# Optimization experiments

Hardware: AMD Instinct MI355X
Metric: run time of the kernel (lower is better)

## Reference

```python
import jax, jax.numpy as jnp
import numpy as np

IN_CH, OUT_CH, HID, NHEAD = 4, 1, 256, 8
VDIM = HID // NHEAD
LOCALITIES = (2.0, 10.0, 10.0, 10.0, 10.0, 200.0)
N_BLOCKS = len(LOCALITIES) - 2
INPUT_RES, LATENT_RES, OUTPUT_RES = (64, 64), (32, 32), (64, 64)
BATCH = 8


def pairwise_dist(res1x, res1y, res2x, res2y):
    gx1 = jnp.linspace(0, 1, res1x + 1)[:-1]
    gy1 = jnp.linspace(0, 1, res1y + 1)[:-1]
    g1x, g1y = jnp.meshgrid(gx1, gy1, indexing='xy')
    grid1 = jnp.stack([g1x.flatten(), g1y.flatten()], axis=-1)
    gx2 = jnp.linspace(0, 1, res2x + 1)[:-1]
    gy2 = jnp.linspace(0, 1, res2y + 1)[:-1]
    g2x, g2y = jnp.meshgrid(gx2, gy2, indexing='xy')
    grid2 = jnp.stack([g2x.flatten(), g2y.flatten()], axis=-1)
    diff = grid1[:, None, :] - grid2[None, :, :]
    return (jnp.sum(diff ** 2, axis=-1) / 2.0).astype(jnp.float32)


def pos_att(m_dist, x, r, w, locality):
    # m_dist:[Nq,Nk]  x:[B,Nk,HID]  r:[H,1,1]  w:[H,HID,VDIM]
    scale = jnp.tan(0.25 * jnp.pi * (1 - 1e-07) * (1 + jnp.sin(r)))
    sd = m_dist[None, :, :] * scale  # [H,Nq,Nk]
    if locality <= 100:
        thr = jnp.percentile(sd, locality, axis=-1, keepdims=True)
        sd = jnp.where(sd <= thr, sd, jnp.inf)
    att = jax.nn.softmax(-sd, axis=-1)  # [H,Nq,Nk]
    value = jnp.einsum('bnj,hjk->bhnk', x, w)  # [B,H,Nk,VDIM]
    out = jnp.einsum('hjn,bhnk->bhjk', att, value)  # [B,H,Nq,VDIM]
    out = jnp.transpose(out, (0, 2, 1, 3)).reshape(x.shape[0], m_dist.shape[0], -1)
    return jax.nn.gelu(out)


def lin(x, w, b):
    # eqx.nn.Linear: w:[out,in], b:[out]
    return jnp.einsum('bni,oi->bno', x, w) + b


def setup_inputs() -> dict:
    key = jax.random.key(0)
    ks = jax.random.split(key, 20)
    Ni = INPUT_RES[0] * INPUT_RES[1]
    s_h = 1.0 / jnp.sqrt(HID)
    s_in = 1.0 / jnp.sqrt(IN_CH)
    return {
        'x': jax.random.normal(ks[0], (BATCH, Ni, IN_CH), jnp.float32),
        'en_fc1_w': jax.random.uniform(ks[1], (HID, IN_CH), jnp.float32, -s_in, s_in),
        'en_fc1_b': jax.random.uniform(ks[2], (HID,), jnp.float32, -s_in, s_in),
        'down_r': jax.random.normal(ks[3], (NHEAD, 1, 1), jnp.float32),
        'down_w': jax.random.normal(ks[4], (NHEAD, HID, VDIM), jnp.float32) * s_h,
        'pa_r': jax.random.normal(ks[5], (N_BLOCKS, NHEAD, 1, 1), jnp.float32),
        'pa_w': jax.random.normal(ks[6], (N_BLOCKS, NHEAD, HID, VDIM), jnp.float32) * s_h,
        'mlp1_w': jax.random.uniform(ks[7], (N_BLOCKS, HID, HID), jnp.float32, -s_h, s_h),
        'mlp1_b': jax.random.uniform(ks[8], (N_BLOCKS, HID), jnp.float32, -s_h, s_h),
        'mlp2_w': jax.random.uniform(ks[9], (N_BLOCKS, HID, HID), jnp.float32, -s_h, s_h),
        'mlp2_b': jax.random.uniform(ks[10], (N_BLOCKS, HID), jnp.float32, -s_h, s_h),
        'res_w': jax.random.uniform(ks[11], (N_BLOCKS, HID, HID), jnp.float32, -s_h, s_h),
        'res_b': jax.random.uniform(ks[12], (N_BLOCKS, HID), jnp.float32, -s_h, s_h),
        'up_r': jax.random.normal(ks[13], (NHEAD, 1, 1), jnp.float32),
        'up_w': jax.random.normal(ks[14], (NHEAD, HID, VDIM), jnp.float32) * s_h,
        'de_fc1_w': jax.random.uniform(ks[15], (HID, HID), jnp.float32, -s_h, s_h),
        'de_fc1_b': jax.random.uniform(ks[16], (HID,), jnp.float32, -s_h, s_h),
        'de_fc2_w': jax.random.uniform(ks[17], (OUT_CH, HID), jnp.float32, -s_h, s_h),
        'de_fc2_b': jax.random.uniform(ks[18], (OUT_CH,), jnp.float32, -s_h, s_h),
    }


def reference(x, en_fc1_w, en_fc1_b, down_r, down_w, pa_r, pa_w,
              mlp1_w, mlp1_b, mlp2_w, mlp2_b, res_w, res_b,
              up_r, up_w, de_fc1_w, de_fc1_b, de_fc2_w, de_fc2_b):
    m_dist_down = pairwise_dist(LATENT_RES[0], LATENT_RES[1], INPUT_RES[0], INPUT_RES[1])
    m_dist_proc = pairwise_dist(LATENT_RES[0], LATENT_RES[1], LATENT_RES[0], LATENT_RES[1])
    m_dist_up = pairwise_dist(OUTPUT_RES[0], OUTPUT_RES[1], LATENT_RES[0], LATENT_RES[1])

    h = jax.nn.gelu(lin(x, en_fc1_w, en_fc1_b))
    h = pos_att(m_dist_down, h, down_r, down_w, LOCALITIES[0])
    for i in range(N_BLOCKS):
        pa_out = pos_att(m_dist_proc, h, pa_r[i], pa_w[i], LOCALITIES[1 + i])
        mlp_out = lin(jax.nn.gelu(lin(pa_out, mlp1_w[i], mlp1_b[i])), mlp2_w[i], mlp2_b[i])
        residual = lin(h, res_w[i], res_b[i])
        h = jax.nn.gelu(mlp_out + residual)
    h = pos_att(m_dist_up, h, up_r, up_w, LOCALITIES[-1])
    h = jax.nn.gelu(lin(h, de_fc1_w, de_fc1_b))
    return lin(h, de_fc2_w, de_fc2_b)
```

## Files before the change

### kernel.cpp

```cpp
#include <hip/hip_runtime.h>
#include <math.h>


#define PI_F 3.14159265358979323846f

typedef __attribute__((ext_vector_type(8))) short short8;
typedef __attribute__((ext_vector_type(4))) float float4v;
typedef __attribute__((ext_vector_type(4))) unsigned short ushort4v;

__device__ __forceinline__ float gelu_f(float x) {
  float u = 0.7978845608028654f * (x + 0.044715f * x * x * x);
  float e = __expf(2.0f * u);
  float t = 1.0f - 2.0f / (e + 1.0f);
  return 0.5f * x * (1.0f + t);
}

__device__ __forceinline__ float head_scale(float r) {
  return tanf(0.25f * PI_F * (1.0f - 1e-7f) * (1.0f + sinf(r)));
}

__device__ __forceinline__ unsigned short f2bf(float f) {
  union { float f; unsigned u; } c; c.f = f;
  unsigned u = c.u + 0x7FFFu + ((c.u >> 16) & 1u);
  return (unsigned short)(u >> 16);
}
__device__ __forceinline__ float bf2f(unsigned short h) {
  union { unsigned u; float f; } c; c.u = ((unsigned)h) << 16;
  return c.f;
}
__device__ __forceinline__ void split_bf(float f, unsigned short& hi,
                                         unsigned short& lo) {
  hi = f2bf(f);
  lo = f2bf(f - bf2f(hi));
}

__global__ __launch_bounds__(256) void k_pre(
    const float* __restrict__ x, const float* __restrict__ en_w,
    const float* __restrict__ en_b, unsigned short* __restrict__ ahi,
    unsigned short* __restrict__ alo, const float* __restrict__ down_w,
    const float* __restrict__ de1_w, const float* __restrict__ up_w,
    const float* __restrict__ pa_w, const float* __restrict__ mlp1_w,
    const float* __restrict__ mlp2_w, const float* __restrict__ res_w,
    unsigned short* __restrict__ whi, unsigned short* __restrict__ wlo,
    float* __restrict__ out, const float* __restrict__ de2_b) {
  int blk = blockIdx.x;
  int tid = threadIdx.x;
  if (blk < 32768) {
    float4 xv = *(const float4*)(x + (size_t)blk * 4);
    float4 wv = *(const float4*)(en_w + (size_t)tid * 4);
    float s = xv.x * wv.x + xv.y * wv.y + xv.z * wv.z + xv.w * wv.w + en_b[tid];
    s = gelu_f(s);
    unsigned short hi, lo;
    split_bf(s, hi, lo);
    ahi[(size_t)blk * 256 + tid] = hi;
    alo[(size_t)blk * 256 + tid] = lo;
  } else if (blk < 37632) {
    int i = (blk - 32768) * 256 + tid;
    float f;
    if (i < 65536) {
      int n = i >> 8, k = i & 255;
      f = down_w[(n >> 5) * 8192 + k * 32 + (n & 31)];
    } else if (i < 131072) {
      f = de1_w[i - 65536];
    } else if (i < 196608) {
      int j = i - 131072;
      int n = j >> 8, k = j & 255;
      f = up_w[(n >> 5) * 8192 + k * 32 + (n & 31)];
    } else if (i < 458752) {
      int j = i - 196608;
      int b2 = j >> 16, r = j & 65535;
      int n = r >> 8, k = r & 255;
      f = pa_w[(size_t)b2 * 65536 + (n >> 5) * 8192 + k * 32 + (n & 31)];
    } else if (i < 720896) {
      f = mlp1_w[i - 458752];
    } else if (i < 983040) {
      f = mlp2_w[i - 720896];
    } else {
      f = res_w[i - 983040];
    }
    unsigned short hi, lo;
    split_bf(f, hi, lo);
    whi[i] = hi;
    wlo[i] = lo;
  } else {
    out[(blk - 37632) * 256 + tid] = de2_b[0];
  }
}

template <int KRES, int CXM, int DSHIFT, int J2, int NPT, int TARGET,
          int ITERS, int TMAX>
__device__ __forceinline__ void klist_body(
    const float* __restrict__ rvec, int* __restrict__ klist2,
    int* __restrict__ kcnt2, float* __restrict__ wlist2, int tile, int tid) {
  __shared__ int cntS;
  __shared__ int sidx[J2];
  __shared__ int sdv[J2][4];
  __shared__ float denS[8][4];
  __shared__ int wsum4[4][4];
  int tx = tile & 15, ty = tile >> 4;
  int cxA[4], cyA[4];
#pragma unroll
  for (int i = 0; i < 4; ++i) {
    int qx = 2 * tx + (i & 1), qy = 2 * ty + (i >> 1);
    cxA[i] = qx * CXM; cyA[i] = qy * CXM;
  }
  int dc[4][NPT];
#pragma unroll
  for (int j = 0; j < NPT; ++j) {
    int p = tid * NPT + j;
    int kx = p & (KRES - 1), ky = p / KRES;
#pragma unroll
    for (int i = 0; i < 4; ++i) {
      int dx = cxA[i] - kx, dy = cyA[i] - ky;
      dc[i][j] = dx * dx + dy * dy;
    }
  }
  int lo4[4] = {0, 0, 0, 0}, hi4[4] = {TMAX, TMAX, TMAX, TMAX};
  for (int it = 0; it < ITERS; ++it) {
    int mid[4], c[4] = {0, 0, 0, 0};
#pragma unroll
    for (int i = 0; i < 4; ++i) {
      mid[i] = (lo4[i] + hi4[i]) >> 1;
      if (lo4[i] < hi4[i]) {
#pragma unroll
        for (int j = 0; j < NPT; ++j) c[i] += (dc[i][j] <= mid[i]) ? 1 : 0;
      }
    }
#pragma unroll
    for (int i = 0; i < 4; ++i)
#pragma unroll
      for (int off = 32; off > 0; off >>= 1)
        c[i] += __shfl_down(c[i], off, 64);
    if ((tid & 63) == 0) {
#pragma unroll
      for (int i = 0; i < 4; ++i) wsum4[tid >> 6][i] = c[i];
    }
    __syncthreads();
#pragma unroll
    for (int i = 0; i < 4; ++i) {
      if (lo4[i] < hi4[i]) {
        int tot = wsum4[0][i] + wsum4[1][i] + wsum4[2][i] + wsum4[3][i];
        if (tot >= TARGET) hi4[i] = mid[i]; else lo4[i] = mid[i] + 1;
      }
    }
    __syncthreads();
  }
  int T[4];
#pragma unroll
  for (int i = 0; i < 4; ++i) T[i] = lo4[i];
  if (tid == 0) cntS = 0;
  __syncthreads();
  int x0 = KRES - 1, x1 = 0, y0 = KRES - 1, y1 = 0;
#pragma unroll
  for (int i = 0; i < 4; ++i) {
    int rad = (int)sqrtf((float)T[i]);
    while ((rad + 1) * (rad + 1) <= T[i]) ++rad;
    while (rad > 0 && rad * rad > T[i]) --rad;
    x0 = min(x0, max(0, cxA[i] - rad));
    x1 = max(x1, min(KRES - 1, cxA[i] + rad));
    y0 = min(y0, max(0, cyA[i] - rad));
    y1 = max(y1, min(KRES - 1, cyA[i] + rad));
  }
  int W = x1 - x0 + 1, H = y1 - y0 + 1, tot = W * H;
  for (int p = tid; p < tot; p += 256) {
    int kx = x0 + p % W, ky = y0 + p / W;
    int d[4]; bool keep = false;
#pragma unroll
    for (int i = 0; i < 4; ++i) {
      int dx = cxA[i] - kx, dy = cyA[i] - ky;
      d[i] = dx * dx + dy * dy;
      keep = keep || (d[i] <= T[i]);
    }
    if (keep) {
      int s = atomicAdd(&cntS, 1);
      if (s < J2) {
        sidx[s] = ky * KRES + kx;
#pragma unroll
        for (int i = 0; i < 4; ++i) sdv[s][i] = d[i];
      }
    }
  }
  __syncthreads();
  int cnt = min(cntS, J2);
  int h = tid >> 5, lane = tid & 31;
  float sc = head_scale(rvec[h]) * (1.0f / (float)(1 << DSHIFT));
  float den[4] = {0.f, 0.f, 0.f, 0.f};
  for (int j = lane; j < cnt; j += 32) {
#pragma unroll
    for (int i = 0; i < 4; ++i)
      if (sdv[j][i] <= T[i]) den[i] += __expf(-sc * (float)sdv[j][i]);
  }
#pragma unroll
  for (int i = 0; i < 4; ++i) {
    float d0 = den[i];
#pragma unroll
    for (int off = 16; off > 0; off >>= 1) d0 += __shfl_down(d0, off, 32);
    if (lane == 0) denS[h][i] = d0;
  }
  __syncthreads();
  float inv[4];
#pragma unroll
  for (int i = 0; i < 4; ++i) inv[i] = 1.0f / denS[h][i];
  for (int j = lane; j < cnt; j += 32) {
    float w[4];
#pragma unroll
    for (int i = 0; i < 4; ++i)
      w[i] = (sdv[j][i] <= T[i]) ? __expf(-sc * (float)sdv[j][i]) * inv[i] : 0.f;
    float4v wv = {w[0], w[1], w[2], w[3]};
    *(float4v*)&wlist2[(((size_t)h * 256 + tile) * J2 + j) * 4] = wv;
  }
  if (tid == 0) kcnt2[tile] = cnt;
  if (h == 0)
    for (int j = lane; j < cnt; j += 32) klist2[(size_t)tile * J2 + j] = sidx[j];
}

__global__ __launch_bounds__(256) void k_klist_all(
    const float* __restrict__ down_r, const float* __restrict__ pa_r,
    int* __restrict__ klD2, int* __restrict__ cntD2, float* __restrict__ wlD2,
    int* __restrict__ klP2, int* __restrict__ cntP2, float* __restrict__ wlP2) {
  int tid = threadIdx.x;
  if (blockIdx.x < 256) {
    klist_body<64, 2, 13, 256, 16, 82, 13, 7938>(down_r, klD2, cntD2, wlD2,
                                                 blockIdx.x, tid);
  } else {
    klist_body<32, 1, 11, 256, 4, 103, 11, 1922>(pa_r, klP2, cntP2, wlP2,
                                                 blockIdx.x - 256, tid);
  }
}

template <int NK, int J2>
__global__ __launch_bounds__(256) void k_att3(
    const float* __restrict__ value,
    const int* __restrict__ klist2, const int* __restrict__ kcnt2,
    const float* __restrict__ wlist2, unsigned short* __restrict__ ohi,
    unsigned short* __restrict__ olo) {
  __shared__ int kls[J2];
  __shared__ float4v wls[J2];
  __shared__ float4v part[4][4][64];
  int blk = blockIdx.x;
  int tile = blk >> 3, h = blk & 7;
  int tid = threadIdx.x, g = tid & 63, s = tid >> 6;
  int cnt = kcnt2[tile];
  for (int j = tid; j < cnt; j += 256) {
    kls[j] = klist2[(size_t)tile * J2 + j];
    wls[j] = *(const float4v*)&wlist2[(((size_t)h * 256 + tile) * J2 + j) * 4];
  }
  __syncthreads();
  const float* vb = value + (size_t)h * NK * 256 + g * 4;
  float4v acc[4];
#pragma unroll
  for (int i = 0; i < 4; ++i) acc[i] = (float4v)0.0f;
  for (int j = s; j < cnt; j += 4) {
    int row = kls[j];
    float4v v = *(const float4v*)(vb + (size_t)row * 256);
    float4v w = wls[j];
    acc[0] += w.x * v;
    acc[1] += w.y * v;
    acc[2] += w.z * v;
    acc[3] += w.w * v;
  }
#pragma unroll
  for (int i = 0; i < 4; ++i) part[s][i][g] = acc[i];
  __syncthreads();
  if (tid < 64) {
    int g2 = tid;
    int ttx = tile & 15, tty = tile >> 4;
    int batch = g2 >> 3, v0 = (g2 & 7) * 4;
#pragma unroll
    for (int i = 0; i < 4; ++i) {
      float4v o4 = part[0][i][g2] + part[1][i][g2] + part[2][i][g2] +
                   part[3][i][g2];
      int q = (2 * tty + (i >> 1)) * 32 + 2 * ttx + (i & 1);
      size_t idx = ((size_t)batch * 1024 + q) * 256 + h * 32 + v0;
      ushort4v hv, lv;
#pragma unroll
      for (int c = 0; c < 4; ++c) {
        float oo = gelu_f(o4[c]);
        unsigned short hi, lo;
        split_bf(oo, hi, lo);
        hv[c] = hi; lv[c] = lo;
      }
      *(ushort4v*)(ohi + idx) = hv;
      *(ushort4v*)(olo + idx) = lv;
    }
  }
}

template <bool DUAL, int OL, bool GEL, bool OHILO>
__global__ __launch_bounds__(256) void k_mf(
    const unsigned short* __restrict__ A1hi, const unsigned short* __restrict__ A1lo,
    const unsigned short* __restrict__ W1hi, const unsigned short* __restrict__ W1lo,
    const unsigned short* __restrict__ A2hi, const unsigned short* __restrict__ A2lo,
    const unsigned short* __restrict__ W2hi, const unsigned short* __restrict__ W2lo,
    const float* __restrict__ bias, const float* __restrict__ bias2,
    float* __restrict__ outf, unsigned short* __restrict__ ohi,
    unsigned short* __restrict__ olo, int NS) {
  __shared__ unsigned short Ah[128][40], Al[128][40];
  __shared__ unsigned short Bh[128][40], Bl[128][40];
  int tid = threadIdx.x;
  int m0 = blockIdx.x * 128, n0 = blockIdx.y * 128;
  int w = tid >> 6, lane = tid & 63;
  int wm = (w >> 1) * 64, wn = (w & 1) * 64;
  int quad = lane >> 4, l16 = lane & 15;
  float4v acc[4][4];
#pragma unroll
  for (int i = 0; i < 4; ++i)
#pragma unroll
    for (int j = 0; j < 4; ++j) acc[i][j] = (float4v)0.0f;

  int srow = tid >> 1, skq = (tid & 1) * 16;
  const int KT = DUAL ? 512 : 256;
  for (int kk = 0; kk < KT; kk += 32) {
    const unsigned short *pAh, *pAl, *pWh, *pWl;
    int kb;
    if (DUAL && kk >= 256) {
      pAh = A2hi; pAl = A2lo; pWh = W2hi; pWl = W2lo; kb = kk - 256;
    } else {
      pAh = A1hi; pAl = A1lo; pWh = W1hi; pWl = W1lo; kb = kk;
    }
    {
      size_t ga = (size_t)(m0 + srow) * 256 + kb + skq;
      const uint4* pah = (const uint4*)(pAh + ga);
      const uint4* pal = (const uint4*)(pAl + ga);
      *(uint4*)&Ah[srow][skq] = pah[0];
      *(uint4*)&Ah[srow][skq + 8] = pah[1];
      *(uint4*)&Al[srow][skq] = pal[0];
      *(uint4*)&Al[srow][skq + 8] = pal[1];
      size_t gb = (size_t)(n0 + srow) * 256 + kb + skq;
      const uint4* pbh = (const uint4*)(pWh + gb);
      const uint4* pbl = (const uint4*)(pWl + gb);
      *(uint4*)&Bh[srow][skq] = pbh[0];
      *(uint4*)&Bh[srow][skq + 8] = pbh[1];
      *(uint4*)&Bl[srow][skq] = pbl[0];
      *(uint4*)&Bl[srow][skq + 8] = pbl[1];
    }
    __syncthreads();
    short8 ah[4], al[4], bh[4], bl[4];
#pragma unroll
    for (int s = 0; s < 4; ++s) {
      ah[s] = *(const short8*)&Ah[wm + s * 16 + l16][quad * 8];
      al[s] = *(const short8*)&Al[wm + s * 16 + l16][quad * 8];
      bh[s] = *(const short8*)&Bh[wn + s * 16 + l16][quad * 8];
      bl[s] = *(const short8*)&Bl[wn + s * 16 + l16][quad * 8];
    }
#pragma unroll
    for (int ms = 0; ms < 4; ++ms)
#pragma unroll
      for (int ns = 0; ns < 4; ++ns) {
        acc[ms][ns] = __builtin_amdgcn_mfma_f32_16x16x32_bf16(
            ah[ms], bh[ns], acc[ms][ns], 0, 0, 0);
        acc[ms][ns] = __builtin_amdgcn_mfma_f32_16x16x32_bf16(
            ah[ms], bl[ns], acc[ms][ns], 0, 0, 0);
        acc[ms][ns] = __builtin_amdgcn_mfma_f32_16x16x32_bf16(
            al[ms], bh[ns], acc[ms][ns], 0, 0, 0);
      }
    __syncthreads();
  }
#pragma unroll
  for (int ms = 0; ms < 4; ++ms) {
#pragma unroll
    for (int ns = 0; ns < 4; ++ns) {
      int n = n0 + wn + ns * 16 + l16;
      float bv = bias ? bias[n] : 0.0f;
      if (DUAL && bias2) bv += bias2[n];
#pragma unroll
      for (int r = 0; r < 4; ++r) {
        int m = m0 + wm + ms * 16 + quad * 4 + r;
        float c = acc[ms][ns][r] + bv;
        if (GEL) c = gelu_f(c);
        if (OHILO) {
          unsigned short chi, clo;
          split_bf(c, chi, clo);
          ohi[(size_t)m * 256 + n] = chi;
          olo[(size_t)m * 256 + n] = clo;
        } else if (OL == 0) {
          outf[(size_t)m * 256 + n] = c;
        } else {
          int N = 1 << NS;
          int bb = m >> NS, rr = m & (N - 1);
          outf[(((size_t)(n >> 5) * N + rr) * 8 + bb) * 32 + (n & 31)] = c;
        }
      }
    }
  }
}

__global__ __launch_bounds__(256) void k_mf_dec(
    const unsigned short* __restrict__ A1hi, const unsigned short* __restrict__ A1lo,
    const unsigned short* __restrict__ W1hi, const unsigned short* __restrict__ W1lo,
    const float* __restrict__ b1, const float* __restrict__ w2,
    float* __restrict__ out) {
  __shared__ unsigned short Ah[128][40], Al[128][40];
  __shared__ unsigned short Bh[128][40], Bl[128][40];
  int tid = threadIdx.x;
  int m0 = blockIdx.x * 128, n0 = blockIdx.y * 128;
  int w = tid >> 6, lane = tid & 63;
  int wm = (w >> 1) * 64, wn = (w & 1) * 64;
  int quad = lane >> 4, l16 = lane & 15;
  float4v acc[4][4];
#pragma unroll
  for (int i = 0; i < 4; ++i)
#pragma unroll
    for (int j = 0; j < 4; ++j) acc[i][j] = (float4v)0.0f;
  int srow = tid >> 1, skq = (tid & 1) * 16;
  for (int kk = 0; kk < 256; kk += 32) {
    {
      size_t ga = (size_t)(m0 + srow) * 256 + kk + skq;
      const uint4* pah = (const uint4*)(A1hi + ga);
      const uint4* pal = (const uint4*)(A1lo + ga);
      *(uint4*)&Ah[srow][skq] = pah[0];
      *(uint4*)&Ah[srow][skq + 8] = pah[1];
      *(uint4*)&Al[srow][skq] = pal[0];
      *(uint4*)&Al[srow][skq + 8] = pal[1];
      size_t gb = (size_t)(n0 + srow) * 256 + kk + skq;
      const uint4* pbh = (const uint4*)(W1hi + gb);
      const uint4* pbl = (const uint4*)(W1lo + gb);
      *(uint4*)&Bh[srow][skq] = pbh[0];
      *(uint4*)&Bh[srow][skq + 8] = pbh[1];
      *(uint4*)&Bl[srow][skq] = pbl[0];
      *(uint4*)&Bl[srow][skq + 8] = pbl[1];
    }
    __syncthreads();
    short8 ah[4], al[4], bh[4], bl[4];
#pragma unroll
    for (int s = 0; s < 4; ++s) {
      ah[s] = *(const short8*)&Ah[wm + s * 16 + l16][quad * 8];
      al[s] = *(const short8*)&Al[wm + s * 16 + l16][quad * 8];
      bh[s] = *(const short8*)&Bh[wn + s * 16 + l16][quad * 8];
      bl[s] = *(const short8*)&Bl[wn + s * 16 + l16][quad * 8];
    }
#pragma unroll
    for (int ms = 0; ms < 4; ++ms)
#pragma unroll
      for (int ns = 0; ns < 4; ++ns) {
        acc[ms][ns] = __builtin_amdgcn_mfma_f32_16x16x32_bf16(
            ah[ms], bh[ns], acc[ms][ns], 0, 0, 0);
        acc[ms][ns] = __builtin_amdgcn_mfma_f32_16x16x32_bf16(
            ah[ms], bl[ns], acc[ms][ns], 0, 0, 0);
        acc[ms][ns] = __builtin_amdgcn_mfma_f32_16x16x32_bf16(
            al[ms], bh[ns], acc[ms][ns], 0, 0, 0);
      }
    __syncthreads();
  }
#pragma unroll
  for (int ms = 0; ms < 4; ++ms) {
#pragma unroll
    for (int r = 0; r < 4; ++r) {
      float p = 0.0f;
#pragma unroll
      for (int ns = 0; ns < 4; ++ns) {
        int n = n0 + wn + ns * 16 + l16;
        float c = gelu_f(acc[ms][ns][r] + b1[n]);
        p += c * w2[n];
      }
      p += __shfl_xor(p, 1, 64);
      p += __shfl_xor(p, 2, 64);
      p += __shfl_xor(p, 4, 64);
      p += __shfl_xor(p, 8, 64);
      if (l16 == 0) {
        int m = m0 + wm + ms * 16 + quad * 4 + r;
        atomicAdd(&out[m], p);
      }
    }
  }
}

template <bool DUAL, int OL, bool GEL, bool OHILO>
__global__ __launch_bounds__(256) void k_mf3(
    const unsigned short* __restrict__ A1hi, const unsigned short* __restrict__ A1lo,
    const unsigned short* __restrict__ W1hi, const unsigned short* __restrict__ W1lo,
    const unsigned short* __restrict__ A2hi, const unsigned short* __restrict__ A2lo,
    const unsigned short* __restrict__ W2hi, const unsigned short* __restrict__ W2lo,
    const float* __restrict__ bias, const float* __restrict__ bias2,
    float* __restrict__ outf, unsigned short* __restrict__ ohi,
    unsigned short* __restrict__ olo, int NS) {
  __shared__ unsigned short Ah[32][40], Al[32][40];
  __shared__ unsigned short Bh[64][40], Bl[64][40];
  int tid = threadIdx.x;
  int m0 = blockIdx.x * 32, n0 = blockIdx.y * 64;
  int w = tid >> 6, lane = tid & 63;
  int wm = (w >> 1) * 16, wn = (w & 1) * 32;
  int quad = lane >> 4, l16 = lane & 15;
  float4v acc[2];
  acc[0] = (float4v)0.0f;
  acc[1] = (float4v)0.0f;
  int sra = tid >> 3, ska = (tid & 7) * 4;
  int srb = tid >> 2, skb = (tid & 3) * 8;
  const int KT = DUAL ? 512 : 256;
  for (int kk = 0; kk < KT; kk += 32) {
    const unsigned short *pAh, *pAl, *pWh, *pWl;
    int kb;
    if (DUAL && kk >= 256) {
      pAh = A2hi; pAl = A2lo; pWh = W2hi; pWl = W2lo; kb = kk - 256;
    } else {
      pAh = A1hi; pAl = A1lo; pWh = W1hi; pWl = W1lo; kb = kk;
    }
    {
      size_t ga = (size_t)(m0 + sra) * 256 + kb + ska;
      *(uint2*)&Ah[sra][ska] = *(const uint2*)(pAh + ga);
      *(uint2*)&Al[sra][ska] = *(const uint2*)(pAl + ga);
      size_t gb = (size_t)(n0 + srb) * 256 + kb + skb;
      *(uint4*)&Bh[srb][skb] = *(const uint4*)(pWh + gb);
      *(uint4*)&Bl[srb][skb] = *(const uint4*)(pWl + gb);
    }
    __syncthreads();
    short8 ah = *(const short8*)&Ah[wm + l16][quad * 8];
    short8 al = *(const short8*)&Al[wm + l16][quad * 8];
#pragma unroll
    for (int ns = 0; ns < 2; ++ns) {
      short8 bh = *(const short8*)&Bh[wn + ns * 16 + l16][quad * 8];
      short8 bl = *(const short8*)&Bl[wn + ns * 16 + l16][quad * 8];
      acc[ns] = __builtin_amdgcn_mfma_f32_16x16x32_bf16(ah, bh, acc[ns], 0, 0, 0);
      acc[ns] = __builtin_amdgcn_mfma_f32_16x16x32_bf16(ah, bl, acc[ns], 0, 0, 0);
      acc[ns] = __builtin_amdgcn_mfma_f32_16x16x32_bf16(al, bh, acc[ns], 0, 0, 0);
    }
    __syncthreads();
  }
#pragma unroll
  for (int ns = 0; ns < 2; ++ns) {
    int n = n0 + wn + ns * 16 + l16;
    float bv = bias ? bias[n] : 0.0f;
    if (DUAL && bias2) bv += bias2[n];
#pragma unroll
    for (int r = 0; r < 4; ++r) {
      int m = m0 + wm + quad * 4 + r;
      float c = acc[ns][r] + bv;
      if (GEL) c = gelu_f(c);
      if (OHILO) {
        unsigned short chi, clo;
        split_bf(c, chi, clo);
        ohi[(size_t)m * 256 + n] = chi;
        olo[(size_t)m * 256 + n] = clo;
      } else if (OL == 0) {
        outf[(size_t)m * 256 + n] = c;
      } else {
        int N = 1 << NS;
        int bb = m >> NS, rr = m & (N - 1);
        outf[(((size_t)(n >> 5) * N + rr) * 8 + bb) * 32 + (n & 31)] = c;
      }
    }
  }
}

__global__ __launch_bounds__(256) void k_up_s1(
    const float* __restrict__ value,
    const float* __restrict__ rvec, float* __restrict__ T) {
  __shared__ float AxL[32][33];
  int ky = blockIdx.x, h = blockIdx.y, qx0 = blockIdx.z * 32;
  int tid = threadIdx.x;
  float sc = head_scale(rvec[h]) * (1.0f / 8192.0f);
  float v[32];
  const float* vb = value + ((size_t)h * 1024 + ky * 32) * 256 + tid;
#pragma unroll
  for (int kx = 0; kx < 32; ++kx) v[kx] = vb[kx * 256];
  if (tid < 32) {
    int qx = qx0 + tid, dxmin = qx & 1;
    for (int kx = 0; kx < 32; ++kx) {
      int dx = qx - 2 * kx;
      AxL[tid][kx] = __expf(-sc * (float)(dx * dx - dxmin));
    }
  }
  __syncthreads();
  for (int qq = 0; qq < 32; ++qq) {
    int qx = qx0 + qq;
    float acc = 0.f;
#pragma unroll
    for (int kx = 0; kx < 32; ++kx) acc += AxL[qq][kx] * v[kx];
    T[(((size_t)h * 64 + qx) * 32 + ky) * 256 + tid] = acc;
  }
}

__global__ __launch_bounds__(256) void k_up_s2(
    const float* __restrict__ T, const float* __restrict__ rvec,
    unsigned short* __restrict__ ohi, unsigned short* __restrict__ olo) {
  __shared__ float AyL[64][33];
  __shared__ float Sy[64];
  __shared__ float SxS;
  int qx = blockIdx.x, h = blockIdx.y, tid = threadIdx.x;
  float sc = head_scale(rvec[h]) * (1.0f / 8192.0f);
  float t[32];
  const float* tb = T + ((size_t)h * 64 + qx) * 32 * 256 + tid;
#pragma unroll
  for (int ky = 0; ky < 32; ++ky) t[ky] = tb[ky * 256];
  if (tid < 64) {
    int qy = tid, dymin = qy & 1;
    float s = 0.f;
    for (int ky = 0; ky < 32; ++ky) {
      int dy = qy - 2 * ky;
      float e = __expf(-sc * (float)(dy * dy - dymin));
      AyL[qy][ky] = e;
      s += e;
    }
    Sy[qy] = s;
  } else if (tid >= 64 && tid < 96) {
    int kx = tid - 64, dxmin = qx & 1;
    int dx = qx - 2 * kx;
    float e = __expf(-sc * (float)(dx * dx - dxmin));
#pragma unroll
    for (int off = 16; off > 0; off >>= 1) e += __shfl_down(e, off, 32);
    if (kx == 0) SxS = e;
  }
  __syncthreads();
  float invSx = 1.0f / SxS;
  int b = tid >> 5, v = tid & 31;
  size_t base = ((size_t)b * 4096 + qx) * 256 + h * 32 + v;
  for (int qy = 0; qy < 64; ++qy) {
    float acc = 0.f;
#pragma unroll
    for (int ky = 0; ky < 32; ++ky) acc += AyL[qy][ky] * t[ky];
    float o = gelu_f(acc * invSx / Sy[qy]);
    unsigned short hi, lo;
    split_bf(o, hi, lo);
    size_t idx = base + (size_t)qy * 64 * 256;
    ohi[idx] = hi;
    olo[idx] = lo;
  }
}

extern "C" void kernel_launch(void* const* d_in, const int* in_sizes, int n_in,
                              void* d_out, int out_size, void* d_ws,
                              size_t ws_size, hipStream_t stream) {
  const float* x      = (const float*)d_in[0];
  const float* en_w   = (const float*)d_in[1];
  const float* en_b   = (const float*)d_in[2];
  const float* down_r = (const float*)d_in[3];
  const float* down_w = (const float*)d_in[4];
  const float* pa_r   = (const float*)d_in[5];
  const float* pa_w   = (const float*)d_in[6];
  const float* mlp1_w = (const float*)d_in[7];
  const float* mlp1_b = (const float*)d_in[8];
  const float* mlp2_w = (const float*)d_in[9];
  const float* mlp2_b = (const float*)d_in[10];
  const float* res_w  = (const float*)d_in[11];
  const float* res_b  = (const float*)d_in[12];
  const float* up_r   = (const float*)d_in[13];
  const float* up_w   = (const float*)d_in[14];
  const float* de1_w  = (const float*)d_in[15];
  const float* de1_b  = (const float*)d_in[16];
  const float* de2_w  = (const float*)d_in[17];
  const float* de2_b  = (const float*)d_in[18];
  float* out = (float*)d_out;

  constexpr int J2 = 256;
  float* ws = (float*)d_ws;
  unsigned short* Ahi = (unsigned short*)ws;
  unsigned short* Alo = Ahi + 8388608;
  float* B = ws + 8388608;
  float* Tbuf = B + 2097152;
  unsigned short* hAhi = (unsigned short*)(ws + 16777216);
  unsigned short* hAlo = hAhi + 2097152;
  unsigned short* hBhi = hAlo + 2097152;
  unsigned short* hBlo = hBhi + 2097152;
  unsigned short* pahi = hBlo + 2097152;
  unsigned short* palo = pahi + 2097152;
  unsigned short* m1hi = palo + 2097152;
  unsigned short* m1lo = m1hi + 2097152;
  int* cntD2 = (int*)(ws + 25165824);
  int* cntP2 = cntD2 + 256;
  int* klD2 = cntP2 + 256;
  int* klP2 = klD2 + 256 * J2;
  float* wlD2 = (float*)(klP2 + 256 * J2);
  float* wlP2 = wlD2 + 2097152;
  unsigned short* Whi = (unsigned short*)(wlP2 + 2097152);
  unsigned short* Wlo = Whi + 1245184;
  const int WO_DOWN = 0, WO_DE1 = 65536, WO_UP = 131072, WO_PA = 196608,
            WO_MLP1 = 458752, WO_MLP2 = 720896, WO_RES = 983040;

  k_pre<<<37760, 256, 0, stream>>>(x, en_w, en_b, Ahi, Alo, down_w, de1_w,
                                   up_w, pa_w, mlp1_w, mlp2_w, res_w, Whi,
                                   Wlo, out, de2_b);
  k_klist_all<<<512, 256, 0, stream>>>(down_r, pa_r, klD2, cntD2, wlD2, klP2,
                                       cntP2, wlP2);
  k_mf<false, 1, false, false><<<dim3(256, 2), 256, 0, stream>>>(
      Ahi, Alo, Whi + WO_DOWN, Wlo + WO_DOWN, nullptr, nullptr, nullptr,
      nullptr, nullptr, nullptr, B, nullptr, nullptr, 12);
  k_att3<4096, J2><<<2048, 256, 0, stream>>>(B, klD2, cntD2, wlD2, hAhi, hAlo);
  for (int i = 0; i < 4; ++i) {
    const unsigned short* hih = (i & 1) ? hBhi : hAhi;
    const unsigned short* hil = (i & 1) ? hBlo : hAlo;
    unsigned short* hoh = (i & 1) ? hAhi : hBhi;
    unsigned short* hol = (i & 1) ? hAlo : hBlo;
    k_mf3<false, 1, false, false><<<dim3(256, 4), 256, 0, stream>>>(
        hih, hil, Whi + WO_PA + i * 65536, Wlo + WO_PA + i * 65536, nullptr,
        nullptr, nullptr, nullptr, nullptr, nullptr, B, nullptr, nullptr, 10);
    k_att3<1024, J2><<<2048, 256, 0, stream>>>(B, klP2, cntP2, wlP2, pahi,
                                               palo);
    k_mf3<false, 0, true, true><<<dim3(256, 4), 256, 0, stream>>>(
        pahi, palo, Whi + WO_MLP1 + i * 65536, Wlo + WO_MLP1 + i * 65536,
        nullptr, nullptr, nullptr, nullptr, mlp1_b + i * 256, nullptr, nullptr,
        m1hi, m1lo, 0);
    k_mf3<true, 0, true, true><<<dim3(256, 4), 256, 0, stream>>>(
        m1hi, m1lo, Whi + WO_MLP2 + i * 65536, Wlo + WO_MLP2 + i * 65536, hih,
        hil, Whi + WO_RES + i * 65536, Wlo + WO_RES + i * 65536,
        mlp2_b + i * 256, res_b + i * 256, nullptr, hoh, hol, 0);
  }
  k_mf3<false, 1, false, false><<<dim3(256, 4), 256, 0, stream>>>(
      hAhi, hAlo, Whi + WO_UP, Wlo + WO_UP, nullptr, nullptr, nullptr, nullptr,
      nullptr, nullptr, B, nullptr, nullptr, 10);
  k_up_s1<<<dim3(32, 8, 2), 256, 0, stream>>>(B, up_r, Tbuf);
  k_up_s2<<<dim3(64, 8), 256, 0, stream>>>(Tbuf, up_r, Ahi, Alo);
  k_mf_dec<<<dim3(256, 2), 256, 0, stream>>>(Ahi, Alo, Whi + WO_DE1,
                                             Wlo + WO_DE1, de1_b, de2_w, out);
}
```

Baseline: 484.9 us.

## Fuse MLP1, MLP2 and residual GEMMs into one kernel; merge klist into k_pre

A new k_mlp kernel computes MLP1 with GELU into shared memory for a 16-row tile, then MLP2 plus the residual linear and the final GELU, all in one launch. This removes the m1 intermediate round-trip through global memory and one launch per block. The klist/softmax-weight construction also moves into extra blocks of k_pre, dropping a separate launch. The cost is small M tiles (16 rows, 512 blocks), so each block reloads the full 256x256 weight matrices three times, which can lower weight reuse and MFMA efficiency compared with the old tiled GEMMs.

```diff
diff --git a/kernel.cpp b/kernel.cpp
--- a/kernel.cpp
+++ b/kernel.cpp
@@ -32,6 +32,133 @@
                                          unsigned short& lo) {
   hi = f2bf(f);
   lo = f2bf(f - bf2f(hi));
+}
+
+template <int KRES, int CXM, int DSHIFT, int J2, int NPT, int TARGET,
+          int ITERS, int TMAX>
+__device__ __forceinline__ void klist_body(
+    const float* __restrict__ rvec, int* __restrict__ klist2,
+    int* __restrict__ kcnt2, float* __restrict__ wlist2, int tile, int tid) {
+  __shared__ int cntS;
+  __shared__ int sidx[J2];
+  __shared__ int sdv[J2][4];
+  __shared__ float denS[8][4];
+  __shared__ int wsum4[4][4];
+  int tx = tile & 15, ty = tile >> 4;
+  int cxA[4], cyA[4];
+#pragma unroll
+  for (int i = 0; i < 4; ++i) {
+    int qx = 2 * tx + (i & 1), qy = 2 * ty + (i >> 1);
+    cxA[i] = qx * CXM; cyA[i] = qy * CXM;
+  }
+  int dc[4][NPT];
+#pragma unroll
+  for (int j = 0; j < NPT; ++j) {
+    int p = tid * NPT + j;
+    int kx = p & (KRES - 1), ky = p / KRES;
+#pragma unroll
+    for (int i = 0; i < 4; ++i) {
+      int dx = cxA[i] - kx, dy = cyA[i] - ky;
+      dc[i][j] = dx * dx + dy * dy;
+    }
+  }
+  int lo4[4] = {0, 0, 0, 0}, hi4[4] = {TMAX, TMAX, TMAX, TMAX};
+  for (int it = 0; it < ITERS; ++it) {
+    int mid[4], c[4] = {0, 0, 0, 0};
+#pragma unroll
+    for (int i = 0; i < 4; ++i) {
+      mid[i] = (lo4[i] + hi4[i]) >> 1;
+      if (lo4[i] < hi4[i]) {
+#pragma unroll
+        for (int j = 0; j < NPT; ++j) c[i] += (dc[i][j] <= mid[i]) ? 1 : 0;
+      }
+    }
+#pragma unroll
+    for (int i = 0; i < 4; ++i)
+#pragma unroll
+      for (int off = 32; off > 0; off >>= 1)
+        c[i] += __shfl_down(c[i], off, 64);
+    if ((tid & 63) == 0) {
+#pragma unroll
+      for (int i = 0; i < 4; ++i) wsum4[tid >> 6][i] = c[i];
+    }
+    __syncthreads();
+#pragma unroll
+    for (int i = 0; i < 4; ++i) {
+      if (lo4[i] < hi4[i]) {
+        int tot = wsum4[0][i] + wsum4[1][i] + wsum4[2][i] + wsum4[3][i];
+        if (tot >= TARGET) hi4[i] = mid[i]; else lo4[i] = mid[i] + 1;
+      }
+    }
+    __syncthreads();
+  }
+  int T[4];
+#pragma unroll
+  for (int i = 0; i < 4; ++i) T[i] = lo4[i];
+  if (tid == 0) cntS = 0;
+  __syncthreads();
+  int x0 = KRES - 1, x1 = 0, y0 = KRES - 1, y1 = 0;
+#pragma unroll
+  for (int i = 0; i < 4; ++i) {
+    int rad = (int)sqrtf((float)T[i]);
+    while ((rad + 1) * (rad + 1) <= T[i]) ++rad;
+    while (rad > 0 && rad * rad > T[i]) --rad;
+    x0 = min(x0, max(0, cxA[i] - rad));
+    x1 = max(x1, min(KRES - 1, cxA[i] + rad));
+    y0 = min(y0, max(0, cyA[i] - rad));
+    y1 = max(y1, min(KRES - 1, cyA[i] + rad));
+  }
+  int W = x1 - x0 + 1, H = y1 - y0 + 1, tot = W * H;
+  for (int p = tid; p < tot; p += 256) {
+    int kx = x0 + p % W, ky = y0 + p / W;
+    int d[4]; bool keep = false;
+#pragma unroll
+    for (int i = 0; i < 4; ++i) {
+      int dx = cxA[i] - kx, dy = cyA[i] - ky;
+      d[i] = dx * dx + dy * dy;
+      keep = keep || (d[i] <= T[i]);
+    }
+    if (keep) {
+      int s = atomicAdd(&cntS, 1);
+      if (s < J2) {
+        sidx[s] = ky * KRES + kx;
+#pragma unroll
+        for (int i = 0; i < 4; ++i) sdv[s][i] = d[i];
+      }
+    }
+  }
+  __syncthreads();
+  int cnt = min(cntS, J2);
+  int h = tid >> 5, lane = tid & 31;
+  float sc = head_scale(rvec[h]) * (1.0f / (float)(1 << DSHIFT));
+  float den[4] = {0.f, 0.f, 0.f, 0.f};
+  for (int j = lane; j < cnt; j += 32) {
+#pragma unroll
+    for (int i = 0; i < 4; ++i)
+      if (sdv[j][i] <= T[i]) den[i] += __expf(-sc * (float)sdv[j][i]);
+  }
+#pragma unroll
+  for (int i = 0; i < 4; ++i) {
+    float d0 = den[i];
+#pragma unroll
+    for (int off = 16; off > 0; off >>= 1) d0 += __shfl_down(d0, off, 32);
+    if (lane == 0) denS[h][i] = d0;
+  }
+  __syncthreads();
+  float inv[4];
+#pragma unroll
+  for (int i = 0; i < 4; ++i) inv[i] = 1.0f / denS[h][i];
+  for (int j = lane; j < cnt; j += 32) {
+    float w[4];
+#pragma unroll
+    for (int i = 0; i < 4; ++i)
+      w[i] = (sdv[j][i] <= T[i]) ? __expf(-sc * (float)sdv[j][i]) * inv[i] : 0.f;
+    float4v wv = {w[0], w[1], w[2], w[3]};
+    *(float4v*)&wlist2[(((size_t)h * 256 + tile) * J2 + j) * 4] = wv;
+  }
+  if (tid == 0) kcnt2[tile] = cnt;
+  if (h == 0)
+    for (int j = lane; j < cnt; j += 32) klist2[(size_t)tile * J2 + j] = sidx[j];
 }
 
 __global__ __launch_bounds__(256) void k_pre(
@@ -42,7 +169,10 @@
     const float* __restrict__ pa_w, const float* __restrict__ mlp1_w,
     const float* __restrict__ mlp2_w, const float* __restrict__ res_w,
     unsigned short* __restrict__ whi, unsigned short* __restrict__ wlo,
-    float* __restrict__ out, const float* __restrict__ de2_b) {
+    float* __restrict__ out, const float* __restrict__ de2_b,
+    const float* __restrict__ down_r, const float* __restrict__ pa_r,
+    int* __restrict__ klD2, int* __restrict__ cntD2, float* __restrict__ wlD2,
+    int* __restrict__ klP2, int* __restrict__ cntP2, float* __restrict__ wlP2) {
   int blk = blockIdx.x;
   int tid = threadIdx.x;
   if (blk < 32768) {
@@ -82,149 +212,14 @@
     split_bf(f, hi, lo);
     whi[i] = hi;
     wlo[i] = lo;
-  } else {
+  } else if (blk < 37760) {
     out[(blk - 37632) * 256 + tid] = de2_b[0];
-  }
-}
-
-template <int KRES, int CXM, int DSHIFT, int J2, int NPT, int TARGET,
-          int ITERS, int TMAX>
-__device__ __forceinline__ void klist_body(
-    const float* __restrict__ rvec, int* __restrict__ klist2,
-    int* __restrict__ kcnt2, float* __restrict__ wlist2, int tile, int tid) {
-  __shared__ int cntS;
-  __shared__ int sidx[J2];
-  __shared__ int sdv[J2][4];
-  __shared__ float denS[8][4];
-  __shared__ int wsum4[4][4];
-  int tx = tile & 15, ty = tile >> 4;
-  int cxA[4], cyA[4];
-#pragma unroll
-  for (int i = 0; i < 4; ++i) {
-    int qx = 2 * tx + (i & 1), qy = 2 * ty + (i >> 1);
-    cxA[i] = qx * CXM; cyA[i] = qy * CXM;
-  }
-  int dc[4][NPT];
-#pragma unroll
-  for (int j = 0; j < NPT; ++j) {
-    int p = tid * NPT + j;
-    int kx = p & (KRES - 1), ky = p / KRES;
-#pragma unroll
-    for (int i = 0; i < 4; ++i) {
-      int dx = cxA[i] - kx, dy = cyA[i] - ky;
-      dc[i][j] = dx * dx + dy * dy;
-    }
-  }
-  int lo4[4] = {0, 0, 0, 0}, hi4[4] = {TMAX, TMAX, TMAX, TMAX};
-  for (int it = 0; it < ITERS; ++it) {
-    int mid[4], c[4] = {0, 0, 0, 0};
-#pragma unroll
-    for (int i = 0; i < 4; ++i) {
-      mid[i] = (lo4[i] + hi4[i]) >> 1;
-      if (lo4[i] < hi4[i]) {
-#pragma unroll
-        for (int j = 0; j < NPT; ++j) c[i] += (dc[i][j] <= mid[i]) ? 1 : 0;
-      }
-    }
-#pragma unroll
-    for (int i = 0; i < 4; ++i)
-#pragma unroll
-      for (int off = 32; off > 0; off >>= 1)
-        c[i] += __shfl_down(c[i], off, 64);
-    if ((tid & 63) == 0) {
-#pragma unroll
-      for (int i = 0; i < 4; ++i) wsum4[tid >> 6][i] = c[i];
-    }
-    __syncthreads();
-#pragma unroll
-    for (int i = 0; i < 4; ++i) {
-      if (lo4[i] < hi4[i]) {
-        int tot = wsum4[0][i] + wsum4[1][i] + wsum4[2][i] + wsum4[3][i];
-        if (tot >= TARGET) hi4[i] = mid[i]; else lo4[i] = mid[i] + 1;
-      }
-    }
-    __syncthreads();
-  }
-  int T[4];
-#pragma unroll
-  for (int i = 0; i < 4; ++i) T[i] = lo4[i];
-  if (tid == 0) cntS = 0;
-  __syncthreads();
-  int x0 = KRES - 1, x1 = 0, y0 = KRES - 1, y1 = 0;
-#pragma unroll
-  for (int i = 0; i < 4; ++i) {
-    int rad = (int)sqrtf((float)T[i]);
-    while ((rad + 1) * (rad + 1) <= T[i]) ++rad;
-    while (rad > 0 && rad * rad > T[i]) --rad;
-    x0 = min(x0, max(0, cxA[i] - rad));
-    x1 = max(x1, min(KRES - 1, cxA[i] + rad));
-    y0 = min(y0, max(0, cyA[i] - rad));
-    y1 = max(y1, min(KRES - 1, cyA[i] + rad));
-  }
-  int W = x1 - x0 + 1, H = y1 - y0 + 1, tot = W * H;
-  for (int p = tid; p < tot; p += 256) {
-    int kx = x0 + p % W, ky = y0 + p / W;
-    int d[4]; bool keep = false;
-#pragma unroll
-    for (int i = 0; i < 4; ++i) {
-      int dx = cxA[i] - kx, dy = cyA[i] - ky;
-      d[i] = dx * dx + dy * dy;
-      keep = keep || (d[i] <= T[i]);
-    }
-    if (keep) {
-      int s = atomicAdd(&cntS, 1);
-      if (s < J2) {
-        sidx[s] = ky * KRES + kx;
-#pragma unroll
-        for (int i = 0; i < 4; ++i) sdv[s][i] = d[i];
-      }
-    }
-  }
-  __syncthreads();
-  int cnt = min(cntS, J2);
-  int h = tid >> 5, lane = tid & 31;
-  float sc = head_scale(rvec[h]) * (1.0f / (float)(1 << DSHIFT));
-  float den[4] = {0.f, 0.f, 0.f, 0.f};
-  for (int j = lane; j < cnt; j += 32) {
-#pragma unroll
-    for (int i = 0; i < 4; ++i)
-      if (sdv[j][i] <= T[i]) den[i] += __expf(-sc * (float)sdv[j][i]);
-  }
-#pragma unroll
-  for (int i = 0; i < 4; ++i) {
-    float d0 = den[i];
-#pragma unroll
-    for (int off = 16; off > 0; off >>= 1) d0 += __shfl_down(d0, off, 32);
-    if (lane == 0) denS[h][i] = d0;
-  }
-  __syncthreads();
-  float inv[4];
-#pragma unroll
-  for (int i = 0; i < 4; ++i) inv[i] = 1.0f / denS[h][i];
-  for (int j = lane; j < cnt; j += 32) {
-    float w[4];
-#pragma unroll
-    for (int i = 0; i < 4; ++i)
-      w[i] = (sdv[j][i] <= T[i]) ? __expf(-sc * (float)sdv[j][i]) * inv[i] : 0.f;
-    float4v wv = {w[0], w[1], w[2], w[3]};
-    *(float4v*)&wlist2[(((size_t)h * 256 + tile) * J2 + j) * 4] = wv;
-  }
-  if (tid == 0) kcnt2[tile] = cnt;
-  if (h == 0)
-    for (int j = lane; j < cnt; j += 32) klist2[(size_t)tile * J2 + j] = sidx[j];
-}
-
-__global__ __launch_bounds__(256) void k_klist_all(
-    const float* __restrict__ down_r, const float* __restrict__ pa_r,
-    int* __restrict__ klD2, int* __restrict__ cntD2, float* __restrict__ wlD2,
-    int* __restrict__ klP2, int* __restrict__ cntP2, float* __restrict__ wlP2) {
-  int tid = threadIdx.x;
-  if (blockIdx.x < 256) {
+  } else if (blk < 38016) {
     klist_body<64, 2, 13, 256, 16, 82, 13, 7938>(down_r, klD2, cntD2, wlD2,
-                                                 blockIdx.x, tid);
+                                                 blk - 37760, tid);
   } else {
     klist_body<32, 1, 11, 256, 4, 103, 11, 1922>(pa_r, klP2, cntP2, wlP2,
-                                                 blockIdx.x - 256, tid);
+                                                 blk - 38016, tid);
   }
 }
 
@@ -542,6 +537,146 @@
   }
 }
 
+__global__ __launch_bounds__(256) void k_mlp(
+    const unsigned short* __restrict__ pahi, const unsigned short* __restrict__ palo,
+    const unsigned short* __restrict__ hhi, const unsigned short* __restrict__ hlo,
+    const unsigned short* __restrict__ W1hi, const unsigned short* __restrict__ W1lo,
+    const unsigned short* __restrict__ W2hi, const unsigned short* __restrict__ W2lo,
+    const unsigned short* __restrict__ Wrhi, const unsigned short* __restrict__ Wrlo,
+    const float* __restrict__ b1, const float* __restrict__ b2,
+    const float* __restrict__ br, unsigned short* __restrict__ ohi,
+    unsigned short* __restrict__ olo) {
+  __shared__ unsigned short Ah[16][40], Al[16][40];
+  __shared__ unsigned short Bh[256][40], Bl[256][40];
+  __shared__ unsigned short M1h[16][264], M1l[16][264];
+  int tid = threadIdx.x;
+  int m0 = blockIdx.x * 16;
+  int w = tid >> 6, lane = tid & 63;
+  int quad = lane >> 4, l16 = lane & 15;
+  int sra = tid >> 4, ska = (tid & 15) * 2;
+  float4v acc[4];
+#pragma unroll
+  for (int i = 0; i < 4; ++i) acc[i] = (float4v)0.0f;
+
+  for (int kk = 0; kk < 256; kk += 32) {
+    {
+      size_t ga = (size_t)(m0 + sra) * 256 + kk + ska;
+      *(unsigned*)&Ah[sra][ska] = *(const unsigned*)(pahi + ga);
+      *(unsigned*)&Al[sra][ska] = *(const unsigned*)(palo + ga);
+      size_t gb = (size_t)tid * 256 + kk;
+      *(uint4*)&Bh[tid][0] = *(const uint4*)(W1hi + gb);
+      *(uint4*)&Bh[tid][8] = *(const uint4*)(W1hi + gb + 8);
+      *(uint4*)&Bh[tid][16] = *(const uint4*)(W1hi + gb + 16);
+      *(uint4*)&Bh[tid][24] = *(const uint4*)(W1hi + gb + 24);
+      *(uint4*)&Bl[tid][0] = *(const uint4*)(W1lo + gb);
+      *(uint4*)&Bl[tid][8] = *(const uint4*)(W1lo + gb + 8);
+      *(uint4*)&Bl[tid][16] = *(const uint4*)(W1lo + gb + 16);
+      *(uint4*)&Bl[tid][24] = *(const uint4*)(W1lo + gb + 24);
+    }
+    __syncthreads();
+    short8 ah = *(const short8*)&Ah[l16][quad * 8];
+    short8 al = *(const short8*)&Al[l16][quad * 8];
+#pragma unroll
+    for (int ns = 0; ns < 4; ++ns) {
+      int nr = w * 64 + ns * 16 + l16;
+      short8 bh = *(const short8*)&Bh[nr][quad * 8];
+      short8 bl = *(const short8*)&Bl[nr][quad * 8];
+      acc[ns] = __builtin_amdgcn_mfma_f32_16x16x32_bf16(ah, bh, acc[ns], 0, 0, 0);
+      acc[ns] = __builtin_amdgcn_mfma_f32_16x16x32_bf16(ah, bl, acc[ns], 0, 0, 0);
+      acc[ns] = __builtin_amdgcn_mfma_f32_16x16x32_bf16(al, bh, acc[ns], 0, 0, 0);
+    }
+    __syncthreads();
+  }
+#pragma unroll
+  for (int ns = 0; ns < 4; ++ns) {
+    int n = w * 64 + ns * 16 + l16;
+    float bv = b1[n];
+#pragma unroll
+    for (int r = 0; r < 4; ++r) {
+      int mr = quad * 4 + r;
+      float c = gelu_f(acc[ns][r] + bv);
+      unsigned short hi, lo;
+      split_bf(c, hi, lo);
+      M1h[mr][n] = hi;
+      M1l[mr][n] = lo;
+    }
+    acc[ns] = (float4v)0.0f;
+  }
+  __syncthreads();
+
+  for (int kk = 0; kk < 256; kk += 32) {
+    {
+      size_t gb = (size_t)tid * 256 + kk;
+      *(uint4*)&Bh[tid][0] = *(const uint4*)(W2hi + gb);
+      *(uint4*)&Bh[tid][8] = *(const uint4*)(W2hi + gb + 8);
+      *(uint4*)&Bh[tid][16] = *(const uint4*)(W2hi + gb + 16);
+      *(uint4*)&Bh[tid][24] = *(const uint4*)(W2hi + gb + 24);
+      *(uint4*)&Bl[tid][0] = *(const uint4*)(W2lo + gb);
+      *(uint4*)&Bl[tid][8] = *(const uint4*)(W2lo + gb + 8);
+      *(uint4*)&Bl[tid][16] = *(const uint4*)(W2lo + gb + 16);
+      *(uint4*)&Bl[tid][24] = *(const uint4*)(W2lo + gb + 24);
+    }
+    __syncthreads();
+    short8 ah = *(const short8*)&M1h[l16][kk + quad * 8];
+    short8 al = *(const short8*)&M1l[l16][kk + quad * 8];
+#pragma unroll
+    for (int ns = 0; ns < 4; ++ns) {
+      int nr = w * 64 + ns * 16 + l16;
+      short8 bh = *(const short8*)&Bh[nr][quad * 8];
+      short8 bl = *(const short8*)&Bl[nr][quad * 8];
+      acc[ns] = __builtin_amdgcn_mfma_f32_16x16x32_bf16(ah, bh, acc[ns], 0, 0, 0);
+      acc[ns] = __builtin_amdgcn_mfma_f32_16x16x32_bf16(ah, bl, acc[ns], 0, 0, 0);
+      acc[ns] = __builtin_amdgcn_mfma_f32_16x16x32_bf16(al, bh, acc[ns], 0, 0, 0);
+    }
+    __syncthreads();
+  }
+
+  for (int kk = 0; kk < 256; kk += 32) {
+    {
+      size_t ga = (size_t)(m0 + sra) * 256 + kk + ska;
+      *(unsigned*)&Ah[sra][ska] = *(const unsigned*)(hhi + ga);
+      *(unsigned*)&Al[sra][ska] = *(const unsigned*)(hlo + ga);
+      size_t gb = (size_t)tid * 256 + kk;
+      *(uint4*)&Bh[tid][0] = *(const uint4*)(Wrhi + gb);
+      *(uint4*)&Bh[tid][8] = *(const uint4*)(Wrhi + gb + 8);
+      *(uint4*)&Bh[tid][16] = *(const uint4*)(Wrhi + gb + 16);
+      *(uint4*)&Bh[tid][24] = *(const uint4*)(Wrhi + gb + 24);
+      *(uint4*)&Bl[tid][0] = *(const uint4*)(Wrlo + gb);
+      *(uint4*)&Bl[tid][8] = *(const uint4*)(Wrlo + gb + 8);
+      *(uint4*)&Bl[tid][16] = *(const uint4*)(Wrlo + gb + 16);
+      *(uint4*)&Bl[tid][24] = *(const uint4*)(Wrlo + gb + 24);
+    }
+    __syncthreads();
+    short8 ah = *(const short8*)&Ah[l16][quad * 8];
+    short8 al = *(const short8*)&Al[l16][quad * 8];
+#pragma unroll
+    for (int ns = 0; ns < 4; ++ns) {
+      int nr = w * 64 + ns * 16 + l16;
+      short8 bh = *(const short8*)&Bh[nr][quad * 8];
+      short8 bl = *(const short8*)&Bl[nr][quad * 8];
+      acc[ns] = __builtin_amdgcn_mfma_f32_16x16x32_bf16(ah, bh, acc[ns], 0, 0, 0);
+      acc[ns] = __builtin_amdgcn_mfma_f32_16x16x32_bf16(ah, bl, acc[ns], 0, 0, 0);
+      acc[ns] = __builtin_amdgcn_mfma_f32_16x16x32_bf16(al, bh, acc[ns], 0, 0, 0);
+    }
+    __syncthreads();
+  }
+
+#pragma unroll
+  for (int ns = 0; ns < 4; ++ns) {
+    int n = w * 64 + ns * 16 + l16;
+    float bv = b2[n] + br[n];
+#pragma unroll
+    for (int r = 0; r < 4; ++r) {
+      int m = m0 + quad * 4 + r;
+      float c = gelu_f(acc[ns][r] + bv);
+      unsigned short hi, lo;
+      split_bf(c, hi, lo);
+      ohi[(size_t)m * 256 + n] = hi;
+      olo[(size_t)m * 256 + n] = lo;
+    }
+  }
+}
+
 __global__ __launch_bounds__(256) void k_up_s1(
     const float* __restrict__ value,
     const float* __restrict__ rvec, float* __restrict__ T) {
@@ -653,8 +788,6 @@
   unsigned short* hBlo = hBhi + 2097152;
   unsigned short* pahi = hBlo + 2097152;
   unsigned short* palo = pahi + 2097152;
-  unsigned short* m1hi = palo + 2097152;
-  unsigned short* m1lo = m1hi + 2097152;
   int* cntD2 = (int*)(ws + 25165824);
   int* cntP2 = cntD2 + 256;
   int* klD2 = cntP2 + 256;
@@ -666,11 +799,10 @@
   const int WO_DOWN = 0, WO_DE1 = 65536, WO_UP = 131072, WO_PA = 196608,
             WO_MLP1 = 458752, WO_MLP2 = 720896, WO_RES = 983040;
 
-  k_pre<<<37760, 256, 0, stream>>>(x, en_w, en_b, Ahi, Alo, down_w, de1_w,
+  k_pre<<<38272, 256, 0, stream>>>(x, en_w, en_b, Ahi, Alo, down_w, de1_w,
                                    up_w, pa_w, mlp1_w, mlp2_w, res_w, Whi,
-                                   Wlo, out, de2_b);
-  k_klist_all<<<512, 256, 0, stream>>>(down_r, pa_r, klD2, cntD2, wlD2, klP2,
-                                       cntP2, wlP2);
+                                   Wlo, out, de2_b, down_r, pa_r, klD2, cntD2,
+                                   wlD2, klP2, cntP2, wlP2);
   k_mf<false, 1, false, false><<<dim3(256, 2), 256, 0, stream>>>(
       Ahi, Alo, Whi + WO_DOWN, Wlo + WO_DOWN, nullptr, nullptr, nullptr,
       nullptr, nullptr, nullptr, B, nullptr, nullptr, 12);
@@ -685,14 +817,12 @@
         nullptr, nullptr, nullptr, nullptr, nullptr, B, nullptr, nullptr, 10);
     k_att3<1024, J2><<<2048, 256, 0, stream>>>(B, klP2, cntP2, wlP2, pahi,
                                                palo);
-    k_mf3<false, 0, true, true><<<dim3(256, 4), 256, 0, stream>>>(
-        pahi, palo, Whi + WO_MLP1 + i * 65536, Wlo + WO_MLP1 + i * 65536,
-        nullptr, nullptr, nullptr, nullptr, mlp1_b + i * 256, nullptr, nullptr,
-        m1hi, m1lo, 0);
-    k_mf3<true, 0, true, true><<<dim3(256, 4), 256, 0, stream>>>(
-        m1hi, m1lo, Whi + WO_MLP2 + i * 65536, Wlo + WO_MLP2 + i * 65536, hih,
-        hil, Whi + WO_RES + i * 65536, Wlo + WO_RES + i * 65536,
-        mlp2_b + i * 256, res_b + i * 256, nullptr, hoh, hol, 0);
+    k_mlp<<<512, 256, 0, stream>>>(
+        pahi, palo, hih, hil, Whi + WO_MLP1 + i * 65536,
+        Wlo + WO_MLP1 + i * 65536, Whi + WO_MLP2 + i * 65536,
+        Wlo + WO_MLP2 + i * 65536, Whi + WO_RES + i * 65536,
+        Wlo + WO_RES + i * 65536, mlp1_b + i * 256, mlp2_b + i * 256,
+        res_b + i * 256, hoh, hol);
   }
   k_mf3<false, 1, false, false><<<dim3(256, 4), 256, 0, stream>>>(
       hAhi, hAlo, Whi + WO_UP, Wlo + WO_UP, nullptr, nullptr, nullptr, nullptr,
```

New measurement: 608.4 us. +25.5%, slower.
